# Optimization experiments

Measured on AMD Instinct MI355X. Metric: run time of the kernel, lower is better.

The kernel has to match this reference:

```python
import jax, jax.numpy as jnp
import numpy as np

E4M3_MAX = 448.0
BLOCK = 128


def _quant_dequant(x, block=BLOCK):
    # x: [R, C] -> block-wise fake-quantized [R, C]
    R, C = x.shape
    pad_r = (-R) % block
    pad_c = (-C) % block
    xp = jnp.pad(x, ((0, pad_r), (0, pad_c)))
    Rp, Cp = R + pad_r, C + pad_c
    # [nR, block, nC, block] -> [nR, nC, block, block]
    xb = xp.reshape(Rp // block, block, Cp // block, block).transpose(0, 2, 1, 3)
    amax = jnp.max(jnp.abs(xb), axis=(-1, -2), keepdims=True)
    scale = jnp.maximum(amax / E4M3_MAX, 1e-8)
    xq = jnp.clip(jnp.round(xb / scale), -E4M3_MAX, E4M3_MAX)
    xdq = (xq * scale).transpose(0, 2, 1, 3).reshape(Rp, Cp)
    return xdq[:R, :C]


def setup_inputs() -> dict:
    key = jax.random.key(0)
    k1, k2 = jax.random.split(key)
    B, S, D_in, D_out = 4, 2048, 4096, 4096
    x = jax.random.normal(k1, (B, S, D_in), dtype=jnp.float32)
    weight = jax.random.normal(k2, (D_out, D_in), dtype=jnp.float32)
    bias = jnp.zeros((D_out,), dtype=jnp.float32)
    return {"x": x, "weight": weight, "bias": bias}


def reference(x, weight, bias):
    batch_shape = x.shape[:-1]
    in_features = x.shape[-1]
    x_flat = x.reshape(-1, in_features)
    x_dq = _quant_dequant(x_flat)
    w_dq = _quant_dequant(weight)
    out = x_dq @ w_dq.T + bias  # [N, out_features]
    return out.reshape(*batch_shape, weight.shape[0])
```

## Files before the change

kernel.cpp:

```cpp
#include <hip/hip_runtime.h>
#include <hip/hip_fp16.h>
#include <stdint.h>

typedef _Float16 half_t;
typedef half_t half8 __attribute__((ext_vector_type(8)));
typedef float f32x4 __attribute__((ext_vector_type(4)));

#define E4M3_MAX 448.0f
#define MFMA16 __builtin_amdgcn_mfma_f32_16x16x32_f16

constexpr int Mdim = 8192, Ndim = 4096, Kdim = 4096;
constexpr int NKT = Kdim / 64;
constexpr int NITER = NKT / 2;
constexpr int NTN = Ndim / 256;
constexpr int NTM = Mdim / 256;
constexpr int LDS_BYTES = 131072;

__global__ __launch_bounds__(256) void quant_kernel(const float* __restrict__ xin,
                                                    const float* __restrict__ win,
                                                    half_t* __restrict__ xq,
                                                    half_t* __restrict__ wq,
                                                    int C) {
    const int cb = blockIdx.x;
    int rb = blockIdx.y;
    const float* in;
    half_t* outq;
    if (rb < Mdim / 128) {
        in = xin; outq = xq;
    } else {
        rb -= Mdim / 128;
        in = win; outq = wq;
    }
    const int tid = threadIdx.x;
    const int col4 = tid & 31;
    const int rsub = tid >> 5;

    const float* base = in + (size_t)(rb * 128 + rsub) * C + cb * 128 + col4 * 4;

    f32x4 v[16];
    float amax = 0.0f;
#pragma unroll
    for (int p = 0; p < 16; ++p) {
        v[p] = *(const f32x4*)(base + (size_t)p * 8 * C);
        amax = fmaxf(amax, fmaxf(fmaxf(fabsf(v[p].x), fabsf(v[p].y)),
                                 fmaxf(fabsf(v[p].z), fabsf(v[p].w))));
    }
#pragma unroll
    for (int off = 32; off > 0; off >>= 1)
        amax = fmaxf(amax, __shfl_xor(amax, off, 64));
    __shared__ float red[4];
    if ((tid & 63) == 0) red[tid >> 6] = amax;
    __syncthreads();
    amax = fmaxf(fmaxf(red[0], red[1]), fmaxf(red[2], red[3]));

    const float scale = fmaxf(amax / E4M3_MAX, 1e-8f);
    const float rs = 1.0f / scale;

    half_t* obase = outq + (size_t)(rb * 128 + rsub) * C + cb * 128 + col4 * 4;
#pragma unroll
    for (int p = 0; p < 16; ++p) {
        float q0 = fminf(fmaxf(rintf(v[p].x * rs), -E4M3_MAX), E4M3_MAX) * scale;
        float q1 = fminf(fmaxf(rintf(v[p].y * rs), -E4M3_MAX), E4M3_MAX) * scale;
        float q2 = fminf(fmaxf(rintf(v[p].z * rs), -E4M3_MAX), E4M3_MAX) * scale;
        float q3 = fminf(fmaxf(rintf(v[p].w * rs), -E4M3_MAX), E4M3_MAX) * scale;
        union { half_t h[4]; uint64_t u; } pk;
        pk.h[0] = (half_t)q0; pk.h[1] = (half_t)q1;
        pk.h[2] = (half_t)q2; pk.h[3] = (half_t)q3;
        *(uint64_t*)(obase + (size_t)p * 8 * C) = pk.u;
    }
}

__device__ __forceinline__ void async16(const half_t* g, char* l) {
    __builtin_amdgcn_global_load_lds((const __attribute__((address_space(1))) void*)g,
                                     (__attribute__((address_space(3))) void*)l, 16, 0, 0);
}

extern __shared__ char smem[];

__global__ __launch_bounds__(512, 2) void gemm_kernel(
    const half_t* __restrict__ A, const half_t* __restrict__ B,
    const float* __restrict__ bias, float* __restrict__ C) {

    const int tid = threadIdx.x;
    const int lane = tid & 63;
    const int wid = tid >> 6;
    const int lo = lane & 15, hi = lane >> 4;
    const int wr = wid >> 2;
    const int wc = wid & 3;

    const int bid = blockIdx.x;
    constexpr int cpx = (NTM * NTN) / 8;
    const int id = (bid & 7) * cpx + (bid >> 3);
    const int tm = id / NTN, tn = id % NTN;

    const int r0 = tid >> 3;
    const int ks = ((tid & 7) ^ (r0 & 7)) * 8;
    const half_t* Abase = A + (size_t)(tm * 256 + r0) * Kdim + ks;
    const half_t* Bbase = B + (size_t)(tn * 256 + r0) * Kdim + ks;
    char* ldstA = smem + tid * 16;
    char* ldstB = smem + 65536 + tid * 16;

#define STG_AS(b, s, kt)                                                                  \
    async16(Abase + (size_t)((s) * 64) * Kdim + (kt) * 64,                                \
            ldstA + (b) * 32768 + (s) * 8192)
#define STG_B(b, h, kt) do {                                                              \
    async16(Bbase + (size_t)((h) * 128) * Kdim + (kt) * 64,                               \
            ldstB + (b) * 32768 + (h) * 16384);                                           \
    async16(Bbase + (size_t)((h) * 128 + 64) * Kdim + (kt) * 64,                          \
            ldstB + (b) * 32768 + (h) * 16384 + 8192); } while (0)

    STG_B(0, 0, 0); STG_B(0, 1, 0);
    STG_AS(0, 0, 0); STG_AS(0, 1, 0); STG_AS(0, 2, 0); STG_AS(0, 3, 0);
    STG_B(1, 0, 1); STG_B(1, 1, 1);
    asm volatile("s_waitcnt vmcnt(4)" ::: "memory");
    __builtin_amdgcn_sched_barrier(0);
    __builtin_amdgcn_s_barrier();
    __builtin_amdgcn_sched_barrier(0);

    const int koff0 = ((hi ^ (lo & 3)) << 4) + (((lo >> 2) & 1) << 6);
    const char* pA0 = smem + wr * 16384 + lo * 128 + koff0;
    const char* pA1 = smem + wr * 16384 + lo * 128 + (koff0 ^ 64);
    const char* pB0 = smem + 65536 + wc * 8192 + lo * 128 + koff0;
    const char* pB1 = smem + 65536 + wc * 8192 + lo * 128 + (koff0 ^ 64);

    f32x4 acc[8][4] = {};
    half8 bfr[4][2];

#define BARSEQ                                                                            \
    __builtin_amdgcn_sched_barrier(0);                                                    \
    __builtin_amdgcn_s_barrier();                                                         \
    __builtin_amdgcn_sched_barrier(0);

#define LDA4(b, q, A00, A01, A10, A11)                                                    \
    half8 A00 = *(const half8*)(pA0 + (b) * 32768 + (q) * 4096);                          \
    half8 A01 = *(const half8*)(pA1 + (b) * 32768 + (q) * 4096);                          \
    half8 A10 = *(const half8*)(pA0 + (b) * 32768 + (q) * 4096 + 2048);                   \
    half8 A11 = *(const half8*)(pA1 + (b) * 32768 + (q) * 4096 + 2048);

#define LDB8(b)                                                                           \
    bfr[0][0] = *(const half8*)(pB0 + (b) * 32768 + 0 * 2048);                            \
    bfr[0][1] = *(const half8*)(pB1 + (b) * 32768 + 0 * 2048);                            \
    bfr[1][0] = *(const half8*)(pB0 + (b) * 32768 + 1 * 2048);                            \
    bfr[1][1] = *(const half8*)(pB1 + (b) * 32768 + 1 * 2048);                            \
    bfr[2][0] = *(const half8*)(pB0 + (b) * 32768 + 2 * 2048);                            \
    bfr[2][1] = *(const half8*)(pB1 + (b) * 32768 + 2 * 2048);                            \
    bfr[3][0] = *(const half8*)(pB0 + (b) * 32768 + 3 * 2048);                            \
    bfr[3][1] = *(const half8*)(pB1 + (b) * 32768 + 3 * 2048);

#define MFMAQ(q, A00, A01, A10, A11)                                                      \
    __builtin_amdgcn_s_setprio(1);                                                        \
    acc[2*(q)][0]   = MFMA16(A00, bfr[0][0], acc[2*(q)][0],   0, 0, 0);                   \
    acc[2*(q)][1]   = MFMA16(A00, bfr[1][0], acc[2*(q)][1],   0, 0, 0);                   \
    acc[2*(q)][2]   = MFMA16(A00, bfr[2][0], acc[2*(q)][2],   0, 0, 0);                   \
    acc[2*(q)][3]   = MFMA16(A00, bfr[3][0], acc[2*(q)][3],   0, 0, 0);                   \
    acc[2*(q)+1][0] = MFMA16(A10, bfr[0][0], acc[2*(q)+1][0], 0, 0, 0);                   \
    acc[2*(q)+1][1] = MFMA16(A10, bfr[1][0], acc[2*(q)+1][1], 0, 0, 0);                   \
    acc[2*(q)+1][2] = MFMA16(A10, bfr[2][0], acc[2*(q)+1][2], 0, 0, 0);                   \
    acc[2*(q)+1][3] = MFMA16(A10, bfr[3][0], acc[2*(q)+1][3], 0, 0, 0);                   \
    acc[2*(q)][0]   = MFMA16(A01, bfr[0][1], acc[2*(q)][0],   0, 0, 0);                   \
    acc[2*(q)][1]   = MFMA16(A01, bfr[1][1], acc[2*(q)][1],   0, 0, 0);                   \
    acc[2*(q)][2]   = MFMA16(A01, bfr[2][1], acc[2*(q)][2],   0, 0, 0);                   \
    acc[2*(q)][3]   = MFMA16(A01, bfr[3][1], acc[2*(q)][3],   0, 0, 0);                   \
    acc[2*(q)+1][0] = MFMA16(A11, bfr[0][1], acc[2*(q)+1][0], 0, 0, 0);                   \
    acc[2*(q)+1][1] = MFMA16(A11, bfr[1][1], acc[2*(q)+1][1], 0, 0, 0);                   \
    acc[2*(q)+1][2] = MFMA16(A11, bfr[2][1], acc[2*(q)+1][2], 0, 0, 0);                   \
    acc[2*(q)+1][3] = MFMA16(A11, bfr[3][1], acc[2*(q)+1][3], 0, 0, 0);                   \
    __builtin_amdgcn_s_setprio(0);

    for (int i = 0; i < NITER; ++i) {
        const int kA1  = 2 * i + 1;
        const int ktn0 = (2 * i + 2) & (NKT - 1);
        const int ktn1 = (2 * i + 3) & (NKT - 1);

        {
            LDB8(0)
            LDA4(0, 0, a00, a01, a10, a11)
            STG_AS(1, 0, kA1); STG_AS(1, 2, kA1);
            asm volatile("s_waitcnt lgkmcnt(8)" ::: "memory");
            BARSEQ
            MFMAQ(0, a00, a01, a10, a11)
        }
        {
            LDA4(0, 1, a00, a01, a10, a11)
            STG_AS(1, 1, kA1); STG_AS(1, 3, kA1);
            BARSEQ
            MFMAQ(1, a00, a01, a10, a11)
        }
        {
            LDA4(0, 2, a00, a01, a10, a11)
            STG_B(0, 0, ktn0);
            BARSEQ
            MFMAQ(2, a00, a01, a10, a11)
        }
        {
            LDA4(0, 3, a00, a01, a10, a11)
            STG_B(0, 1, ktn0);
            asm volatile("s_waitcnt vmcnt(4)" ::: "memory");
            BARSEQ
            MFMAQ(3, a00, a01, a10, a11)
        }
        {
            LDB8(1)
            LDA4(1, 0, a00, a01, a10, a11)
            STG_AS(0, 0, ktn0); STG_AS(0, 2, ktn0);
            asm volatile("s_waitcnt lgkmcnt(8)" ::: "memory");
            BARSEQ
            MFMAQ(0, a00, a01, a10, a11)
        }
        {
            LDA4(1, 1, a00, a01, a10, a11)
            STG_AS(0, 1, ktn0); STG_AS(0, 3, ktn0);
            BARSEQ
            MFMAQ(1, a00, a01, a10, a11)
        }
        {
            LDA4(1, 2, a00, a01, a10, a11)
            STG_B(1, 0, ktn1);
            BARSEQ
            MFMAQ(2, a00, a01, a10, a11)
        }
        {
            LDA4(1, 3, a00, a01, a10, a11)
            STG_B(1, 1, ktn1);
            asm volatile("s_waitcnt vmcnt(4)" ::: "memory");
            BARSEQ
            MFMAQ(3, a00, a01, a10, a11)
        }
    }

    asm volatile("s_waitcnt vmcnt(0)" ::: "memory");

    const int rbase = tm * 256 + wr * 128;
    const int cbase = tn * 256 + wc * 64;
    float bv0 = bias[cbase + 0 * 16 + lo];
    float bv1 = bias[cbase + 1 * 16 + lo];
    float bv2 = bias[cbase + 2 * 16 + lo];
    float bv3 = bias[cbase + 3 * 16 + lo];
#pragma unroll
    for (int m = 0; m < 8; ++m) {
        const int r0r = rbase + m * 16 + hi * 4;
#pragma unroll
        for (int r = 0; r < 4; ++r) {
            float* crow = C + (size_t)(r0r + r) * Ndim + cbase + lo;
            crow[0]  = acc[m][0][r] + bv0;
            crow[16] = acc[m][1][r] + bv1;
            crow[32] = acc[m][2][r] + bv2;
            crow[48] = acc[m][3][r] + bv3;
        }
    }
}

extern "C" void kernel_launch(void* const* d_in, const int* in_sizes, int n_in,
                              void* d_out, int out_size, void* d_ws, size_t ws_size,
                              hipStream_t stream) {
    const float* x = (const float*)d_in[0];
    const float* w = (const float*)d_in[1];
    const float* bias = (const float*)d_in[2];
    float* out = (float*)d_out;

    if (in_sizes[2] != Ndim || in_sizes[1] != Ndim * Kdim || in_sizes[0] != Mdim * Kdim)
        return;

    const size_t xq_bytes = (size_t)Mdim * Kdim * sizeof(half_t);
    const size_t wq_bytes = (size_t)Ndim * Kdim * sizeof(half_t);
    if (ws_size < xq_bytes + wq_bytes) return;

    half_t* xq = (half_t*)d_ws;
    half_t* wq = (half_t*)((char*)d_ws + xq_bytes);

    quant_kernel<<<dim3(Kdim / 128, Mdim / 128 + Ndim / 128), 256, 0, stream>>>(
        x, w, xq, wq, Kdim);

    (void)hipFuncSetAttribute((const void*)gemm_kernel,
                              hipFuncAttributeMaxDynamicSharedMemorySize, LDS_BYTES);

    gemm_kernel<<<dim3(NTM * NTN), dim3(512), LDS_BYTES, stream>>>(xq, wq, bias, out);
}
```

Measured before the change: 274.1 us.

## Double-buffer A fragments in registers to overlap LDS reads with MFMA

Restructures the main GEMM loop so the A-fragment LDS reads for the next quarter-step are issued before the MFMAs of the current quarter, using two alternating register sets (ax/ay) plus a prologue and a peeled tail. This aims to hide LDS read latency behind matrix-core work instead of waiting on lgkmcnt before each MFMA block. The explicit lgkmcnt waits are removed and the compiler is left to insert them, and the extra live registers may raise VGPR pressure.

```diff
diff --git a/kernel.cpp b/kernel.cpp
--- a/kernel.cpp
+++ b/kernel.cpp
@@ -125,17 +125,19 @@
 
     f32x4 acc[8][4] = {};
     half8 bfr[4][2];
+    half8 ax0, ax1, ax2, ax3;
+    half8 ay0, ay1, ay2, ay3;
 
 #define BARSEQ                                                                            \
     __builtin_amdgcn_sched_barrier(0);                                                    \
     __builtin_amdgcn_s_barrier();                                                         \
     __builtin_amdgcn_sched_barrier(0);
 
-#define LDA4(b, q, A00, A01, A10, A11)                                                    \
-    half8 A00 = *(const half8*)(pA0 + (b) * 32768 + (q) * 4096);                          \
-    half8 A01 = *(const half8*)(pA1 + (b) * 32768 + (q) * 4096);                          \
-    half8 A10 = *(const half8*)(pA0 + (b) * 32768 + (q) * 4096 + 2048);                   \
-    half8 A11 = *(const half8*)(pA1 + (b) * 32768 + (q) * 4096 + 2048);
+#define LDA4(b, q, R0, R1, R2, R3)                                                        \
+    R0 = *(const half8*)(pA0 + (b) * 32768 + (q) * 4096);                                 \
+    R1 = *(const half8*)(pA1 + (b) * 32768 + (q) * 4096);                                 \
+    R2 = *(const half8*)(pA0 + (b) * 32768 + (q) * 4096 + 2048);                          \
+    R3 = *(const half8*)(pA1 + (b) * 32768 + (q) * 4096 + 2048);
 
 #define LDB8(b)                                                                           \
     bfr[0][0] = *(const half8*)(pB0 + (b) * 32768 + 0 * 2048);                            \
@@ -167,64 +169,55 @@
     acc[2*(q)+1][3] = MFMA16(A11, bfr[3][1], acc[2*(q)+1][3], 0, 0, 0);                   \
     __builtin_amdgcn_s_setprio(0);
 
+    LDB8(0)
+    LDA4(0, 0, ax0, ax1, ax2, ax3)
+    STG_AS(1, 0, 1); STG_AS(1, 2, 1);
+    BARSEQ
+
     for (int i = 0; i < NITER; ++i) {
         const int kA1  = 2 * i + 1;
         const int ktn0 = (2 * i + 2) & (NKT - 1);
         const int ktn1 = (2 * i + 3) & (NKT - 1);
 
-        {
+        LDA4(0, 1, ay0, ay1, ay2, ay3)
+        MFMAQ(0, ax0, ax1, ax2, ax3)
+        STG_AS(1, 1, kA1); STG_AS(1, 3, kA1);
+        BARSEQ
+        LDA4(0, 2, ax0, ax1, ax2, ax3)
+        MFMAQ(1, ay0, ay1, ay2, ay3)
+        STG_B(0, 0, ktn0);
+        BARSEQ
+        LDA4(0, 3, ay0, ay1, ay2, ay3)
+        MFMAQ(2, ax0, ax1, ax2, ax3)
+        STG_B(0, 1, ktn0);
+        asm volatile("s_waitcnt vmcnt(4)" ::: "memory");
+        BARSEQ
+        LDA4(1, 0, ax0, ax1, ax2, ax3)
+        MFMAQ(3, ay0, ay1, ay2, ay3)
+        LDB8(1)
+        STG_AS(0, 0, ktn0); STG_AS(0, 2, ktn0);
+        BARSEQ
+        LDA4(1, 1, ay0, ay1, ay2, ay3)
+        MFMAQ(0, ax0, ax1, ax2, ax3)
+        STG_AS(0, 1, ktn0); STG_AS(0, 3, ktn0);
+        BARSEQ
+        LDA4(1, 2, ax0, ax1, ax2, ax3)
+        MFMAQ(1, ay0, ay1, ay2, ay3)
+        STG_B(1, 0, ktn1);
+        BARSEQ
+        LDA4(1, 3, ay0, ay1, ay2, ay3)
+        MFMAQ(2, ax0, ax1, ax2, ax3)
+        STG_B(1, 1, ktn1);
+        asm volatile("s_waitcnt vmcnt(4)" ::: "memory");
+        BARSEQ
+        if (i + 1 < NITER) {
+            LDA4(0, 0, ax0, ax1, ax2, ax3)
+            MFMAQ(3, ay0, ay1, ay2, ay3)
             LDB8(0)
-            LDA4(0, 0, a00, a01, a10, a11)
-            STG_AS(1, 0, kA1); STG_AS(1, 2, kA1);
-            asm volatile("s_waitcnt lgkmcnt(8)" ::: "memory");
+            STG_AS(1, 0, 2 * i + 3); STG_AS(1, 2, 2 * i + 3);
             BARSEQ
-            MFMAQ(0, a00, a01, a10, a11)
-        }
-        {
-            LDA4(0, 1, a00, a01, a10, a11)
-            STG_AS(1, 1, kA1); STG_AS(1, 3, kA1);
-            BARSEQ
-            MFMAQ(1, a00, a01, a10, a11)
-        }
-        {
-            LDA4(0, 2, a00, a01, a10, a11)
-            STG_B(0, 0, ktn0);
-            BARSEQ
-            MFMAQ(2, a00, a01, a10, a11)
-        }
-        {
-            LDA4(0, 3, a00, a01, a10, a11)
-            STG_B(0, 1, ktn0);
-            asm volatile("s_waitcnt vmcnt(4)" ::: "memory");
-            BARSEQ
-            MFMAQ(3, a00, a01, a10, a11)
-        }
-        {
-            LDB8(1)
-            LDA4(1, 0, a00, a01, a10, a11)
-            STG_AS(0, 0, ktn0); STG_AS(0, 2, ktn0);
-            asm volatile("s_waitcnt lgkmcnt(8)" ::: "memory");
-            BARSEQ
-            MFMAQ(0, a00, a01, a10, a11)
-        }
-        {
-            LDA4(1, 1, a00, a01, a10, a11)
-            STG_AS(0, 1, ktn0); STG_AS(0, 3, ktn0);
-            BARSEQ
-            MFMAQ(1, a00, a01, a10, a11)
-        }
-        {
-            LDA4(1, 2, a00, a01, a10, a11)
-            STG_B(1, 0, ktn1);
-            BARSEQ
-            MFMAQ(2, a00, a01, a10, a11)
-        }
-        {
-            LDA4(1, 3, a00, a01, a10, a11)
-            STG_B(1, 1, ktn1);
-            asm volatile("s_waitcnt vmcnt(4)" ::: "memory");
-            BARSEQ
-            MFMAQ(3, a00, a01, a10, a11)
+        } else {
+            MFMAQ(3, ay0, ay1, ay2, ay3)
         }
     }
 
```

After: 280.2 us. 1.02x slower.
